# Kernel optimization log

Measured on AMD Instinct MI355X. Metric: run time of the kernel, lower is better.

## Reference

```python
import math
import jax, jax.numpy as jnp
import numpy as np

SCALE = 1.0
OFFSET = 0.0
B, D, R = 524288, 64, 256


def setup_inputs() -> dict:
    key = jax.random.key(0)
    k1, k2, k3 = jax.random.split(key, 3)
    y = jax.random.uniform(k1, (B, 1), dtype=jnp.float32)  # in [0,1)
    x = jax.random.normal(k2, (B, D), dtype=jnp.float32)
    W = jax.random.normal(k3, (D, R), dtype=jnp.float32) * 0.05
    b = jnp.zeros((R,), dtype=jnp.float32)
    logdet = jnp.zeros((B,), dtype=jnp.float32)
    base_points = jnp.linspace(0.0, 1.0, R, dtype=jnp.float32)
    return {"y": y, "x": x, "W": W, "b": b, "logdet": logdet, "base_points": base_points}


def reference(y, x, W, b, logdet, base_points):
    # f(x): linear layer -> [B, R] logits; softmax + cumsum gives monotone CDF-like features
    basefeatures = jnp.cumsum(jax.nn.softmax(x @ W + b, axis=1), axis=1)  # [B, R]
    # bucketize: number of boundaries <= y, minus 1  == searchsorted(side='right') - 1
    start = jnp.searchsorted(base_points, y[:, 0], side="right") - 1  # [B] in [0, R-2]
    i = jnp.arange(basefeatures.shape[0])
    x0 = base_points[start][:, None]            # [B,1]
    x1 = base_points[start + 1][:, None]        # [B,1]
    f0 = basefeatures[i, start][:, None]        # [B,1]
    f1 = basefeatures[i, start + 1][:, None]    # [B,1]
    slope = (f1 - f0) / (x1 - x0)               # [B,1]
    z = SCALE * (f0 + slope * (y - x0)) + OFFSET
    dlogdet = math.log(SCALE) + jnp.log(jnp.abs(slope[:, 0]))
    return z, x, logdet + dlogdet
```

## Files before the change

kernel.cpp:

```cpp
#include <hip/hip_runtime.h>
#include <hip/hip_bf16.h>


#define NB 524288
#define NWT (NB / 16)

typedef __attribute__((ext_vector_type(4))) float f32x4;
typedef __attribute__((ext_vector_type(4))) unsigned int u32x4;
typedef __attribute__((ext_vector_type(8))) __bf16 bf16x8;

#define LOG2E 1.4426950408889634f

static __device__ __forceinline__ unsigned short f2b(float f) {
    unsigned u = __builtin_bit_cast(unsigned, f);
    u += 0x7fffu + ((u >> 16) & 1u);
    return (unsigned short)(u >> 16);
}
static __device__ __forceinline__ unsigned pk2t(float a, float b) {
    return (__builtin_bit_cast(unsigned, a) >> 16) | (__builtin_bit_cast(unsigned, b) & 0xffff0000u);
}

__global__ __launch_bounds__(512, 4) void interp1d_kernel(
    const float* __restrict__ y, const float* __restrict__ x,
    const float* __restrict__ W, const float* __restrict__ bias,
    const float* __restrict__ logdet, const float* __restrict__ bp,
    float* __restrict__ out)
{
    __shared__ unsigned short sW[2 * 16 * 64 * 8];
    __shared__ float sBP[256];
    __shared__ float sBias[256];

    const int t = threadIdx.x;

    if (t < 256) {
        sBP[t]   = bp[t];
        sBias[t] = bias[t] * LOG2E;
    }
    {
        const int col = t & 255;
        const int k0  = (t >> 8) << 5;
        const int lane16lo = col & 15;
        const int n = col >> 4;
        for (int kk = 0; kk < 32; ++kk) {
            int k = k0 + kk;
            float wv = W[k * 256 + col] * LOG2E;
            int lane16 = ((k >> 3) & 3) * 16 + lane16lo;
            int kb = k >> 5, i = k & 7;
            sW[((kb * 16 + n) * 64 + lane16) * 8 + i] = f2b(wv);
        }
    }
    __syncthreads();

    const int lane = t & 63;
    const int colb = lane & 15;
    const int kH   = lane >> 4;
    const int nw   = gridDim.x << 3;

    int wt = (blockIdx.x << 3) | (t >> 6);

    f32x4 v0 = {}, v1 = {}, v2 = {}, v3 = {};
    float yv = 0.f, ldv = 0.f;
    if (wt < NWT) {
        const float* xr = x + (size_t)((wt << 4) + colb) * 64 + (kH << 3);
        v0 = *reinterpret_cast<const f32x4*>(xr);
        v1 = *reinterpret_cast<const f32x4*>(xr + 4);
        v2 = *reinterpret_cast<const f32x4*>(xr + 32);
        v3 = *reinterpret_cast<const f32x4*>(xr + 36);
        yv  = y[(wt << 4) + colb];
        ldv = logdet[(wt << 4) + colb];
    }

    for (; wt < NWT; wt += nw) {
        const int m0 = wt << 4;
        const int wtn = wt + nw;

        f32x4 n0 = {}, n1 = {}, n2 = {}, n3 = {};
        float yn = 0.f, ldn = 0.f;
        if (wtn < NWT) {
            const float* xr = x + (size_t)((wtn << 4) + colb) * 64 + (kH << 3);
            n0 = *reinterpret_cast<const f32x4*>(xr);
            n1 = *reinterpret_cast<const f32x4*>(xr + 4);
            n2 = *reinterpret_cast<const f32x4*>(xr + 32);
            n3 = *reinterpret_cast<const f32x4*>(xr + 36);
            yn  = y[(wtn << 4) + colb];
            ldn = logdet[(wtn << 4) + colb];
        }

        asm volatile("" ::: "memory");

        float* xo = out + NB + (size_t)(m0 + colb) * 64 + (kH << 3);
        *reinterpret_cast<f32x4*>(xo)      = v0;
        *reinterpret_cast<f32x4*>(xo + 4)  = v1;
        *reinterpret_cast<f32x4*>(xo + 32) = v2;
        *reinterpret_cast<f32x4*>(xo + 36) = v3;

        u32x4 pa, pb;
        pa[0] = pk2t(v0[0], v0[1]); pa[1] = pk2t(v0[2], v0[3]);
        pa[2] = pk2t(v1[0], v1[1]); pa[3] = pk2t(v1[2], v1[3]);
        pb[0] = pk2t(v2[0], v2[1]); pb[1] = pk2t(v2[2], v2[3]);
        pb[2] = pk2t(v3[0], v3[1]); pb[3] = pk2t(v3[2], v3[3]);
        bf16x8 a0 = __builtin_bit_cast(bf16x8, pa);
        bf16x8 a1 = __builtin_bit_cast(bf16x8, pb);

        int s = (int)floorf(yv * 255.0f);
        s = min(254, max(0, s));
        s += (sBP[s + 1] <= yv) ? 1 : 0;
        s = min(s, 254);
        s -= (sBP[s] > yv) ? 1 : 0;
        s = max(s, 0);

        const int sb  = s >> 4,  so  = s & 15;
        const int sb1 = (s + 1) >> 4, so1 = (s + 1) & 15;
        float m[4], pm[4];
        #pragma unroll
        for (int j = 0; j < 4; ++j) {
            m[j]  = ((kH << 2) + j <= so)  ? 1.f : 0.f;
            pm[j] = ((kH << 2) + j == so1) ? 1.f : 0.f;
        }

        float denom = 0.f, f0s = 0.f, p1 = 0.f;
        #pragma unroll
        for (int n = 0; n < 16; ++n) {
            bf16x8 w0 = *reinterpret_cast<const bf16x8*>(&sW[(n * 64 + lane) * 8]);
            bf16x8 w1 = *reinterpret_cast<const bf16x8*>(&sW[((16 + n) * 64 + lane) * 8]);
            f32x4 c = *reinterpret_cast<const f32x4*>(&sBias[(n << 4) + (kH << 2)]);
            c = __builtin_amdgcn_mfma_f32_16x16x32_bf16(w0, a0, c, 0, 0, 0);
            c = __builtin_amdgcn_mfma_f32_16x16x32_bf16(w1, a1, c, 0, 0, 0);
            float e0 = __builtin_amdgcn_exp2f(c[0]);
            float e1 = __builtin_amdgcn_exp2f(c[1]);
            float e2 = __builtin_amdgcn_exp2f(c[2]);
            float e3 = __builtin_amdgcn_exp2f(c[3]);
            float bs = (e0 + e1) + (e2 + e3);
            denom += bs;
            float t0 = fmaf(e3, m[3], fmaf(e2, m[2], fmaf(e1, m[1], e0 * m[0])));
            float tp = fmaf(e3, pm[3], fmaf(e2, pm[2], fmaf(e1, pm[1], e0 * pm[0])));
            f0s += (n < sb) ? bs : ((n == sb) ? t0 : 0.f);
            p1  += (n == sb1) ? tp : 0.f;
        }

        denom += __shfl_xor(denom, 16, 64);
        f0s   += __shfl_xor(f0s,   16, 64);
        p1    += __shfl_xor(p1,    16, 64);
        denom += __shfl_xor(denom, 32, 64);
        f0s   += __shfl_xor(f0s,   32, 64);
        p1    += __shfl_xor(p1,    32, 64);

        if (kH == 0) {
            float x0 = sBP[s], x1 = sBP[s + 1];
            float inv = 1.0f / denom;
            float f0 = f0s * inv;
            float slope = (p1 * inv) / (x1 - x0);
            out[m0 + colb] = fmaf(slope, yv - x0, f0);
            out[(size_t)NB * 65 + m0 + colb] = ldv + __logf(fabsf(slope));
        }

        if (wtn < NWT) {
            v0 = n0; v1 = n1; v2 = n2; v3 = n3;
            yv = yn; ldv = ldn;
        }
    }
}

extern "C" void kernel_launch(void* const* d_in, const int* in_sizes, int n_in,
                              void* d_out, int out_size, void* d_ws, size_t ws_size,
                              hipStream_t stream) {
    (void)in_sizes; (void)n_in; (void)out_size; (void)d_ws; (void)ws_size;
    const float* y      = (const float*)d_in[0];
    const float* x      = (const float*)d_in[1];
    const float* W      = (const float*)d_in[2];
    const float* b      = (const float*)d_in[3];
    const float* logdet = (const float*)d_in[4];
    const float* bp     = (const float*)d_in[5];
    float* out = (float*)d_out;
    interp1d_kernel<<<dim3(1024), dim3(512), 0, stream>>>(y, x, W, b, logdet, bp, out);
}
```

Baseline: 64.17 us.

## Process two tiles per MFMA pass and issue input loads before LDS setup

Replaces the grid-stride loop with a fixed schedule in which each wave handles four 16-row tiles, processed two at a time, so MFMA and exp work from independent tiles can interleave. Loads of the first two tiles are issued before the shared-memory W/bias staging, which hides global latency behind the setup. The next pair's loads are issued before computing the current pair. The bf16 packing now uses a single byte-permute instruction, and occupancy is reduced to 2 blocks per CU to allow more registers. The kernel hardcodes 1024 blocks × 8 waves × 4 tiles covering exactly NB rows, with no bounds checks.

```diff
diff --git a/kernel.cpp b/kernel.cpp
--- a/kernel.cpp
+++ b/kernel.cpp
@@ -4,6 +4,7 @@
 
 #define NB 524288
 #define NWT (NB / 16)
+#define NWAVES 8192
 
 typedef __attribute__((ext_vector_type(4))) float f32x4;
 typedef __attribute__((ext_vector_type(4))) unsigned int u32x4;
@@ -17,10 +18,138 @@
     return (unsigned short)(u >> 16);
 }
 static __device__ __forceinline__ unsigned pk2t(float a, float b) {
-    return (__builtin_bit_cast(unsigned, a) >> 16) | (__builtin_bit_cast(unsigned, b) & 0xffff0000u);
-}
-
-__global__ __launch_bounds__(512, 4) void interp1d_kernel(
+    return __builtin_amdgcn_perm(__builtin_bit_cast(unsigned, b),
+                                 __builtin_bit_cast(unsigned, a), 0x07060302u);
+}
+
+struct TState {
+    bf16x8 a0, a1;
+    float yv, ldv;
+    float m[4], pm[4];
+    int s;
+    int m0;
+};
+
+static __device__ __forceinline__ TState stage1(
+    int wt, f32x4 v0, f32x4 v1, f32x4 v2, f32x4 v3, float yv, float ldv,
+    int colb, int kH, const float* sBP, float* out)
+{
+    TState st;
+    st.m0 = wt << 4; st.yv = yv; st.ldv = ldv;
+
+    float* xo = out + NB + (size_t)(st.m0 + colb) * 64 + (kH << 3);
+    *reinterpret_cast<f32x4*>(xo)      = v0;
+    *reinterpret_cast<f32x4*>(xo + 4)  = v1;
+    *reinterpret_cast<f32x4*>(xo + 32) = v2;
+    *reinterpret_cast<f32x4*>(xo + 36) = v3;
+
+    u32x4 pa, pb;
+    pa[0] = pk2t(v0[0], v0[1]); pa[1] = pk2t(v0[2], v0[3]);
+    pa[2] = pk2t(v1[0], v1[1]); pa[3] = pk2t(v1[2], v1[3]);
+    pb[0] = pk2t(v2[0], v2[1]); pb[1] = pk2t(v2[2], v2[3]);
+    pb[2] = pk2t(v3[0], v3[1]); pb[3] = pk2t(v3[2], v3[3]);
+    st.a0 = __builtin_bit_cast(bf16x8, pa);
+    st.a1 = __builtin_bit_cast(bf16x8, pb);
+
+    int s = (int)floorf(yv * 255.0f);
+    s = min(254, max(0, s));
+    s += (sBP[s + 1] <= yv) ? 1 : 0;
+    s = min(s, 254);
+    s -= (sBP[s] > yv) ? 1 : 0;
+    s = max(s, 0);
+    st.s = s;
+
+    const int so  = s & 15;
+    const int so1 = (s + 1) & 15;
+    #pragma unroll
+    for (int j = 0; j < 4; ++j) {
+        st.m[j]  = ((kH << 2) + j <= so)  ? 1.f : 0.f;
+        st.pm[j] = ((kH << 2) + j == so1) ? 1.f : 0.f;
+    }
+    return st;
+}
+
+static __device__ __forceinline__ void stage2_pair(
+    const TState& A, const TState& B, int lane, int colb, int kH,
+    const unsigned short* sW, const float* sBP, const float* sBias, float* out)
+{
+    const int sbA = A.s >> 4, sbA1 = (A.s + 1) >> 4;
+    const int sbB = B.s >> 4, sbB1 = (B.s + 1) >> 4;
+
+    float dA = 0.f, fA = 0.f, pA = 0.f;
+    float dB = 0.f, fB = 0.f, pB = 0.f;
+    #pragma unroll
+    for (int n = 0; n < 16; ++n) {
+        bf16x8 w0 = *reinterpret_cast<const bf16x8*>(&sW[(n * 64 + lane) * 8]);
+        bf16x8 w1 = *reinterpret_cast<const bf16x8*>(&sW[((16 + n) * 64 + lane) * 8]);
+        f32x4 bi = *reinterpret_cast<const f32x4*>(&sBias[(n << 4) + (kH << 2)]);
+
+        f32x4 cA = __builtin_amdgcn_mfma_f32_16x16x32_bf16(w0, A.a0, bi, 0, 0, 0);
+        cA = __builtin_amdgcn_mfma_f32_16x16x32_bf16(w1, A.a1, cA, 0, 0, 0);
+        f32x4 cB = __builtin_amdgcn_mfma_f32_16x16x32_bf16(w0, B.a0, bi, 0, 0, 0);
+        cB = __builtin_amdgcn_mfma_f32_16x16x32_bf16(w1, B.a1, cB, 0, 0, 0);
+
+        {
+            float e0 = __builtin_amdgcn_exp2f(cA[0]);
+            float e1 = __builtin_amdgcn_exp2f(cA[1]);
+            float e2 = __builtin_amdgcn_exp2f(cA[2]);
+            float e3 = __builtin_amdgcn_exp2f(cA[3]);
+            float bs = (e0 + e1) + (e2 + e3);
+            dA += bs;
+            float t0 = fmaf(e3, A.m[3], fmaf(e2, A.m[2], fmaf(e1, A.m[1], e0 * A.m[0])));
+            float tp = fmaf(e3, A.pm[3], fmaf(e2, A.pm[2], fmaf(e1, A.pm[1], e0 * A.pm[0])));
+            fA += (n < sbA) ? bs : ((n == sbA) ? t0 : 0.f);
+            pA += (n == sbA1) ? tp : 0.f;
+        }
+        {
+            float e0 = __builtin_amdgcn_exp2f(cB[0]);
+            float e1 = __builtin_amdgcn_exp2f(cB[1]);
+            float e2 = __builtin_amdgcn_exp2f(cB[2]);
+            float e3 = __builtin_amdgcn_exp2f(cB[3]);
+            float bs = (e0 + e1) + (e2 + e3);
+            dB += bs;
+            float t0 = fmaf(e3, B.m[3], fmaf(e2, B.m[2], fmaf(e1, B.m[1], e0 * B.m[0])));
+            float tp = fmaf(e3, B.pm[3], fmaf(e2, B.pm[2], fmaf(e1, B.pm[1], e0 * B.pm[0])));
+            fB += (n < sbB) ? bs : ((n == sbB) ? t0 : 0.f);
+            pB += (n == sbB1) ? tp : 0.f;
+        }
+    }
+
+    dA += __shfl_xor(dA, 16, 64); fA += __shfl_xor(fA, 16, 64); pA += __shfl_xor(pA, 16, 64);
+    dA += __shfl_xor(dA, 32, 64); fA += __shfl_xor(fA, 32, 64); pA += __shfl_xor(pA, 32, 64);
+    dB += __shfl_xor(dB, 16, 64); fB += __shfl_xor(fB, 16, 64); pB += __shfl_xor(pB, 16, 64);
+    dB += __shfl_xor(dB, 32, 64); fB += __shfl_xor(fB, 32, 64); pB += __shfl_xor(pB, 32, 64);
+
+    if (kH == 0) {
+        {
+            float x0 = sBP[A.s], x1 = sBP[A.s + 1];
+            float inv = 1.0f / dA;
+            float slope = (pA * inv) / (x1 - x0);
+            out[A.m0 + colb] = fmaf(slope, A.yv - x0, fA * inv);
+            out[(size_t)NB * 65 + A.m0 + colb] = A.ldv + __logf(fabsf(slope));
+        }
+        {
+            float x0 = sBP[B.s], x1 = sBP[B.s + 1];
+            float inv = 1.0f / dB;
+            float slope = (pB * inv) / (x1 - x0);
+            out[B.m0 + colb] = fmaf(slope, B.yv - x0, fB * inv);
+            out[(size_t)NB * 65 + B.m0 + colb] = B.ldv + __logf(fabsf(slope));
+        }
+    }
+}
+
+#define LOADT(wt, v0, v1, v2, v3, yv, ldv)                                     \
+    {                                                                          \
+        const float* xr = x + (size_t)(((wt) << 4) + colb) * 64 + (kH << 3);   \
+        v0 = *reinterpret_cast<const f32x4*>(xr);                              \
+        v1 = *reinterpret_cast<const f32x4*>(xr + 4);                          \
+        v2 = *reinterpret_cast<const f32x4*>(xr + 32);                         \
+        v3 = *reinterpret_cast<const f32x4*>(xr + 36);                         \
+        yv  = y[((wt) << 4) + colb];                                           \
+        ldv = logdet[((wt) << 4) + colb];                                      \
+    }
+
+__global__ __launch_bounds__(512, 2) void interp1d_kernel(
     const float* __restrict__ y, const float* __restrict__ x,
     const float* __restrict__ W, const float* __restrict__ bias,
     const float* __restrict__ logdet, const float* __restrict__ bp,
@@ -31,6 +160,15 @@
     __shared__ float sBias[256];
 
     const int t = threadIdx.x;
+    const int lane = t & 63;
+    const int colb = lane & 15;
+    const int kH   = lane >> 4;
+    const int wid  = (blockIdx.x << 3) | (t >> 6);
+
+    f32x4 A0, A1, A2, A3, B0, B1, B2, B3;
+    float yA, lA, yB, lB;
+    LOADT(wid,          A0, A1, A2, A3, yA, lA);
+    LOADT(wid + NWAVES, B0, B1, B2, B3, yB, lB);
 
     if (t < 256) {
         sBP[t]   = bp[t];
@@ -51,114 +189,22 @@
     }
     __syncthreads();
 
-    const int lane = t & 63;
-    const int colb = lane & 15;
-    const int kH   = lane >> 4;
-    const int nw   = gridDim.x << 3;
-
-    int wt = (blockIdx.x << 3) | (t >> 6);
-
-    f32x4 v0 = {}, v1 = {}, v2 = {}, v3 = {};
-    float yv = 0.f, ldv = 0.f;
-    if (wt < NWT) {
-        const float* xr = x + (size_t)((wt << 4) + colb) * 64 + (kH << 3);
-        v0 = *reinterpret_cast<const f32x4*>(xr);
-        v1 = *reinterpret_cast<const f32x4*>(xr + 4);
-        v2 = *reinterpret_cast<const f32x4*>(xr + 32);
-        v3 = *reinterpret_cast<const f32x4*>(xr + 36);
-        yv  = y[(wt << 4) + colb];
-        ldv = logdet[(wt << 4) + colb];
-    }
-
-    for (; wt < NWT; wt += nw) {
-        const int m0 = wt << 4;
-        const int wtn = wt + nw;
-
-        f32x4 n0 = {}, n1 = {}, n2 = {}, n3 = {};
-        float yn = 0.f, ldn = 0.f;
-        if (wtn < NWT) {
-            const float* xr = x + (size_t)((wtn << 4) + colb) * 64 + (kH << 3);
-            n0 = *reinterpret_cast<const f32x4*>(xr);
-            n1 = *reinterpret_cast<const f32x4*>(xr + 4);
-            n2 = *reinterpret_cast<const f32x4*>(xr + 32);
-            n3 = *reinterpret_cast<const f32x4*>(xr + 36);
-            yn  = y[(wtn << 4) + colb];
-            ldn = logdet[(wtn << 4) + colb];
-        }
-
-        asm volatile("" ::: "memory");
-
-        float* xo = out + NB + (size_t)(m0 + colb) * 64 + (kH << 3);
-        *reinterpret_cast<f32x4*>(xo)      = v0;
-        *reinterpret_cast<f32x4*>(xo + 4)  = v1;
-        *reinterpret_cast<f32x4*>(xo + 32) = v2;
-        *reinterpret_cast<f32x4*>(xo + 36) = v3;
-
-        u32x4 pa, pb;
-        pa[0] = pk2t(v0[0], v0[1]); pa[1] = pk2t(v0[2], v0[3]);
-        pa[2] = pk2t(v1[0], v1[1]); pa[3] = pk2t(v1[2], v1[3]);
-        pb[0] = pk2t(v2[0], v2[1]); pb[1] = pk2t(v2[2], v2[3]);
-        pb[2] = pk2t(v3[0], v3[1]); pb[3] = pk2t(v3[2], v3[3]);
-        bf16x8 a0 = __builtin_bit_cast(bf16x8, pa);
-        bf16x8 a1 = __builtin_bit_cast(bf16x8, pb);
-
-        int s = (int)floorf(yv * 255.0f);
-        s = min(254, max(0, s));
-        s += (sBP[s + 1] <= yv) ? 1 : 0;
-        s = min(s, 254);
-        s -= (sBP[s] > yv) ? 1 : 0;
-        s = max(s, 0);
-
-        const int sb  = s >> 4,  so  = s & 15;
-        const int sb1 = (s + 1) >> 4, so1 = (s + 1) & 15;
-        float m[4], pm[4];
-        #pragma unroll
-        for (int j = 0; j < 4; ++j) {
-            m[j]  = ((kH << 2) + j <= so)  ? 1.f : 0.f;
-            pm[j] = ((kH << 2) + j == so1) ? 1.f : 0.f;
-        }
-
-        float denom = 0.f, f0s = 0.f, p1 = 0.f;
-        #pragma unroll
-        for (int n = 0; n < 16; ++n) {
-            bf16x8 w0 = *reinterpret_cast<const bf16x8*>(&sW[(n * 64 + lane) * 8]);
-            bf16x8 w1 = *reinterpret_cast<const bf16x8*>(&sW[((16 + n) * 64 + lane) * 8]);
-            f32x4 c = *reinterpret_cast<const f32x4*>(&sBias[(n << 4) + (kH << 2)]);
-            c = __builtin_amdgcn_mfma_f32_16x16x32_bf16(w0, a0, c, 0, 0, 0);
-            c = __builtin_amdgcn_mfma_f32_16x16x32_bf16(w1, a1, c, 0, 0, 0);
-            float e0 = __builtin_amdgcn_exp2f(c[0]);
-            float e1 = __builtin_amdgcn_exp2f(c[1]);
-            float e2 = __builtin_amdgcn_exp2f(c[2]);
-            float e3 = __builtin_amdgcn_exp2f(c[3]);
-            float bs = (e0 + e1) + (e2 + e3);
-            denom += bs;
-            float t0 = fmaf(e3, m[3], fmaf(e2, m[2], fmaf(e1, m[1], e0 * m[0])));
-            float tp = fmaf(e3, pm[3], fmaf(e2, pm[2], fmaf(e1, pm[1], e0 * pm[0])));
-            f0s += (n < sb) ? bs : ((n == sb) ? t0 : 0.f);
-            p1  += (n == sb1) ? tp : 0.f;
-        }
-
-        denom += __shfl_xor(denom, 16, 64);
-        f0s   += __shfl_xor(f0s,   16, 64);
-        p1    += __shfl_xor(p1,    16, 64);
-        denom += __shfl_xor(denom, 32, 64);
-        f0s   += __shfl_xor(f0s,   32, 64);
-        p1    += __shfl_xor(p1,    32, 64);
-
-        if (kH == 0) {
-            float x0 = sBP[s], x1 = sBP[s + 1];
-            float inv = 1.0f / denom;
-            float f0 = f0s * inv;
-            float slope = (p1 * inv) / (x1 - x0);
-            out[m0 + colb] = fmaf(slope, yv - x0, f0);
-            out[(size_t)NB * 65 + m0 + colb] = ldv + __logf(fabsf(slope));
-        }
-
-        if (wtn < NWT) {
-            v0 = n0; v1 = n1; v2 = n2; v3 = n3;
-            yv = yn; ldv = ldn;
-        }
-    }
+    TState sA = stage1(wid,          A0, A1, A2, A3, yA, lA, colb, kH, sBP, out);
+    TState sB = stage1(wid + NWAVES, B0, B1, B2, B3, yB, lB, colb, kH, sBP, out);
+
+    f32x4 C0, C1, C2, C3, D0, D1, D2, D3;
+    float yC, lC, yD, lD;
+    LOADT(wid + 2 * NWAVES, C0, C1, C2, C3, yC, lC);
+    LOADT(wid + 3 * NWAVES, D0, D1, D2, D3, yD, lD);
+
+    asm volatile("" ::: "memory");
+    stage2_pair(sA, sB, lane, colb, kH, sW, sBP, sBias, out);
+
+    asm volatile("" ::: "memory");
+
+    TState sC = stage1(wid + 2 * NWAVES, C0, C1, C2, C3, yC, lC, colb, kH, sBP, out);
+    TState sD = stage1(wid + 3 * NWAVES, D0, D1, D2, D3, yD, lD, colb, kH, sBP, out);
+    stage2_pair(sC, sD, lane, colb, kH, sW, sBP, sBias, out);
 }
 
 extern "C" void kernel_launch(void* const* d_in, const int* in_sizes, int n_in,
```

After: 67.40 us. +5.0%, slower.
